# Kernel optimization log

Hardware: AMD Instinct MI355X
Metric: run time of the kernel (lower is better)

The kernel has to match this reference:

```python
import jax, jax.numpy as jnp
import numpy as np

N = 500000
TOL = 0.01
ALPHA = 0.1
SLOPE = 0.01
EPS = 1e-10


def smooth_relu(x):
    # 0 for x<0; x^2/2 for 0<=x<1; x-1/2 for x>=1 (C1 smooth ReLU)
    return jnp.where(x < 0, 0.0, jnp.where(x < 1, 0.5 * x * x, x - 0.5))


def leaky_relu(x):
    return jnp.where(x >= 0, x, SLOPE * x)


def _xavier(key, shape):
    fan_out, fan_in = shape
    std = np.sqrt(2.0 / (fan_in + fan_out)).astype(np.float32)
    return jax.random.normal(key, shape, dtype=jnp.float32) * std


def setup_inputs() -> dict:
    key = jax.random.key(0)
    ks = jax.random.split(key, 16)
    inp = {
        'X': jax.random.normal(ks[0], (N, 2), dtype=jnp.float32),
        'Xstable': jnp.zeros((N, 2), dtype=jnp.float32),
        'Vl1_w': _xavier(ks[1], (64, 2)),
        'V2x_w': _xavier(ks[2], (64, 2)),
        'V2z_w': _xavier(ks[3], (64, 64)),
        'V3x_w': _xavier(ks[4], (64, 2)),
        'V3z_w': _xavier(ks[5], (64, 64)),
        'Vfx_w': _xavier(ks[6], (1, 2)),
        'Vfz_w': _xavier(ks[7], (1, 64)),
        'f1_w': _xavier(ks[8], (128, 2)),
        'f1_b': jnp.zeros((128,), dtype=jnp.float32),
        'f2_w': _xavier(ks[9], (128, 128)),
        'f2_b': jnp.zeros((128,), dtype=jnp.float32),
        'f3_w': _xavier(ks[10], (128, 128)),
        'f3_b': jnp.zeros((128,), dtype=jnp.float32),
        'f4_w': _xavier(ks[11], (128, 128)),
        'f4_b': jnp.zeros((128,), dtype=jnp.float32),
        'f5_w': _xavier(ks[12], (128, 128)),
        'f5_b': jnp.zeros((128,), dtype=jnp.float32),
        'ff_w': _xavier(ks[13], (2, 128)),
        'ff_b': jnp.zeros((2,), dtype=jnp.float32),
    }
    return inp


def _V_forward(X, Xstable, Vl1_w, V2x_w, V2z_w, V3x_w, V3z_w, Vfx_w, Vfz_w):
    d = X - Xstable                                  # [N,2]
    z1 = smooth_relu(d @ Vl1_w.T)                    # [N,64]
    z2 = smooth_relu(d @ V2x_w.T + z1 @ V2z_w.T)     # [N,64]
    z3 = smooth_relu(d @ V3x_w.T + z2 @ V3z_w.T)     # [N,64]
    zf = smooth_relu(d @ Vfx_w.T + z3 @ Vfz_w.T)     # [N,1]
    vsum = TOL * jnp.sum(d * d, axis=1, keepdims=True)
    return smooth_relu(zf) + vsum                    # [N,1]


def _fhat_forward(X, f1_w, f1_b, f2_w, f2_b, f3_w, f3_b, f4_w, f4_b, f5_w, f5_b, ff_w, ff_b):
    h = leaky_relu(X @ f1_w.T + f1_b)
    h = leaky_relu(h @ f2_w.T + f2_b)
    h = leaky_relu(h @ f3_w.T + f3_b)
    h = leaky_relu(h @ f4_w.T + f4_b)
    h = leaky_relu(h @ f5_w.T + f5_b)
    return h @ ff_w.T + ff_b                         # [N,2]


def reference(X, Xstable, Vl1_w, V2x_w, V2z_w, V3x_w, V3z_w, Vfx_w, Vfz_w,
              f1_w, f1_b, f2_w, f2_b, f3_w, f3_b, f4_w, f4_b, f5_w, f5_b, ff_w, ff_b):
    def Vfn(Xv):
        return _V_forward(Xv, Xstable, Vl1_w, V2x_w, V2z_w, V3x_w, V3z_w, Vfx_w, Vfz_w)

    V, pullback = jax.vjp(Vfn, X)
    gradV = pullback(jnp.ones_like(V))[0]            # dV/dX, [N,2]

    f_hat = _fhat_forward(X, f1_w, f1_b, f2_w, f2_b, f3_w, f3_b,
                          f4_w, f4_b, f5_w, f5_b, ff_w, ff_b)

    Vnorm = jnp.sum(gradV * gradV, axis=1, keepdims=True)      # [N,1]
    fh_V = jnp.sum(f_hat * gradV, axis=1, keepdims=True)       # [N,1]
    f_mul = jax.nn.relu(fh_V + ALPHA * V) / (Vnorm + EPS)      # [N,1]
    f = f_hat - gradV * f_mul                                  # [N,2]
    return f
```

## Files before the change

### kernel.cpp

```cpp
#include <hip/hip_runtime.h>


typedef _Float16 v2h __attribute__((ext_vector_type(2)));
typedef __fp16   v2hf __attribute__((ext_vector_type(2)));
typedef _Float16 v4h __attribute__((ext_vector_type(4)));
typedef _Float16 v8h __attribute__((ext_vector_type(8)));
typedef float    v4f __attribute__((ext_vector_type(4)));

__device__ __forceinline__ v2h cvt_pk(float a, float b){
  v2hf r = __builtin_amdgcn_cvt_pkrtz(a, b);
  union { v2hf f; v2h h; } u; u.f = r;
  return u.h;
}

#define NPTS 500000
#define FH_BLK  ((NPTS + 127) / 128)
#define VN_BLK  ((NPTS + 127) / 128)
#define FUSED_GRID (FH_BLK + VN_BLK)

#define OFF_FW    0
#define OFF_V2Z   65536
#define OFF_V3Z   69632
#define OFF_V2ZT  73728
#define OFF_V3ZT  77824
#define OFF_VL1T  81920
#define OFF_V2XT  82048
#define OFF_V3XT  82176
#define OFF_VFZ   82304
#define OFF_FFW   82368
#define OFF_F1W   82624
#define W16_DATA  82880
#define W16_TOTAL (W16_DATA + 2048)

__device__ __align__(16) _Float16 g_w16[W16_TOTAL];
__device__ __align__(16) float    g_fh[NPTS * 2];
__device__ __align__(16) float4   g_grad[NPTS];

#if defined(__has_builtin)
#if __has_builtin(__builtin_amdgcn_fdot2)
#define FDOT2(a,b,c) __builtin_amdgcn_fdot2((a),(b),(c),false)
#endif
#endif
#ifndef FDOT2
__device__ __forceinline__ float fdot2_fb(v2h a, v2h b, float c){
  return fmaf((float)a.x, (float)b.x, fmaf((float)a.y, (float)b.y, c));
}
#define FDOT2(a,b,c) fdot2_fb((a),(b),(c))
#endif

__device__ __forceinline__ float srelu(float x){
  float c = fminf(fmaxf(x, 0.f), 1.f);
  return c * fmaf(-0.5f, c, x);
}
__device__ __forceinline__ float sreluD(float x){
  return fminf(fmaxf(x, 0.f), 1.f);
}
__device__ __forceinline__ float sreluD_from_z(float z){
  return fminf(sqrtf(2.f * z), 1.f);
}
__device__ __forceinline__ float dot8(v8h a, v8h b, float s){
  const v2h* ap = (const v2h*)&a;
  const v2h* bp = (const v2h*)&b;
  s = FDOT2(ap[0], bp[0], s);
  s = FDOT2(ap[1], bp[1], s);
  s = FDOT2(ap[2], bp[2], s);
  s = FDOT2(ap[3], bp[3], s);
  return s;
}

__device__ __forceinline__ v2h lrelu_pk(float a, float b){
  v2h x = cvt_pk(a, b);
  v2h m = x * (v2h){(_Float16)0.01f, (_Float16)0.01f};
  return __builtin_elementwise_max(x, m);
}
__device__ __forceinline__ v2h srelu_pk(float a, float b){
  v2h x = cvt_pk(a, b);
  const v2h z0 = (v2h){(_Float16)0.f, (_Float16)0.f};
  const v2h o1 = (v2h){(_Float16)1.f, (_Float16)1.f};
  const v2h hf = (v2h){(_Float16)0.5f, (_Float16)0.5f};
  v2h c = __builtin_elementwise_min(__builtin_elementwise_max(x, z0), o1);
  v2h t = x - c * hf;
  return c * t;
}

__global__ __launch_bounds__(256) void prep_kernel(
  const float* __restrict__ f2w, const float* __restrict__ f3w,
  const float* __restrict__ f4w, const float* __restrict__ f5w,
  const float* __restrict__ V2z, const float* __restrict__ V3z,
  const float* __restrict__ Vl1, const float* __restrict__ V2x,
  const float* __restrict__ V3x, const float* __restrict__ Vfz,
  const float* __restrict__ ffw, const float* __restrict__ f1w)
{
  const int i = blockIdx.x * 256 + threadIdx.x;
  if (i >= W16_TOTAL) return;
  if (i >= W16_DATA){ g_w16[i] = (_Float16)0.f; return; }
  float v;
  if (i < 65536){
    const float* W[4] = {f2w, f3w, f4w, f5w};
    v = W[i >> 14][i & 16383];
  } else if (i < 69632)  v = V2z[i - 65536];
  else if (i < 73728)    v = V3z[i - 69632];
  else if (i < 77824){ int r = i - 73728; v = V2z[(r & 63)*64 + (r >> 6)]; }
  else if (i < 81920){ int r = i - 77824; v = V3z[(r & 63)*64 + (r >> 6)]; }
  else if (i < 82048){ int r = i - 81920; v = Vl1[(r & 63)*2 + (r >> 6)]; }
  else if (i < 82176){ int r = i - 82048; v = V2x[(r & 63)*2 + (r >> 6)]; }
  else if (i < 82304){ int r = i - 82176; v = V3x[(r & 63)*2 + (r >> 6)]; }
  else if (i < 82368)    v = Vfz[i - 82304];
  else if (i < 82624)    v = ffw[i - 82368];
  else                   v = f1w[i - 82624];
  g_w16[i] = (_Float16)v;
}

__device__ __forceinline__ void fh_layer(_Float16* H,
    const _Float16* __restrict__ Wl, const float* __restrict__ Bp,
    int w, int lm, int q)
{
  v4f acc[2][8];
#pragma unroll
  for (int mt = 0; mt < 2; ++mt)
#pragma unroll
    for (int nt = 0; nt < 8; ++nt) acc[mt][nt] = (v4f){0.f,0.f,0.f,0.f};

#pragma unroll
  for (int kt = 0; kt < 4; ++kt){
    const int sw = ((kt*4 + q) ^ lm) << 3;
    v8h A0 = *(const v8h*)(Wl + (w*32      + lm)*128 + kt*32 + q*8);
    v8h A1 = *(const v8h*)(Wl + (w*32 + 16 + lm)*128 + kt*32 + q*8);
#pragma unroll
    for (int nt = 0; nt < 8; ++nt){
      v8h B = *(const v8h*)(H + (nt*16 + lm)*128 + sw);
      acc[0][nt] = __builtin_amdgcn_mfma_f32_16x16x32_f16(A0, B, acc[0][nt], 0,0,0);
      acc[1][nt] = __builtin_amdgcn_mfma_f32_16x16x32_f16(A1, B, acc[1][nt], 0,0,0);
    }
  }
  __syncthreads();
#pragma unroll
  for (int mt = 0; mt < 2; ++mt){
    const int o0 = w*32 + mt*16 + q*4;
    const v4f bv = *(const v4f*)(Bp + o0);
    const int coff = (((o0 >> 3) ^ lm) << 3) + (o0 & 7);
#pragma unroll
    for (int nt = 0; nt < 8; ++nt){
      v4h hv;
      *(v2h*)&hv       = lrelu_pk(acc[mt][nt][0] + bv[0], acc[mt][nt][1] + bv[1]);
      *((v2h*)&hv + 1) = lrelu_pk(acc[mt][nt][2] + bv[2], acc[mt][nt][3] + bv[3]);
      *(v4h*)(H + (nt*16 + lm)*128 + coff) = hv;
    }
  }
  __syncthreads();
}

__device__ __forceinline__ void fhat_body(int b, _Float16* H,
  const float* __restrict__ X,
  const float* __restrict__ f1b, const float* __restrict__ f2b,
  const float* __restrict__ f3b, const float* __restrict__ f4b,
  const float* __restrict__ f5b, const float* __restrict__ ffb)
{
  const int t  = threadIdx.x;
  const int w  = t >> 6;
  const int l  = t & 63;
  const int lm = l & 15;
  const int q  = l >> 4;

  {
    const int r = t >> 1, hf = t & 1, rsw = r & 15;
    int g = b*128 + r; if (g > NPTS-1) g = NPTS-1;
    const float2 xv = *(const float2*)(X + g*2);
    v2h xh; xh.x = (_Float16)xv.x; xh.y = (_Float16)xv.y;
#pragma unroll
    for (int c8 = 0; c8 < 8; ++c8){
      const int c = hf*8 + c8;
      const v4f b0 = *(const v4f*)(f1b + c*8);
      const v4f b1 = *(const v4f*)(f1b + c*8 + 4);
      float vv[8];
#pragma unroll
      for (int j = 0; j < 8; ++j){
        const v2h wv = *(const v2h*)(g_w16 + OFF_F1W + (c*8 + j)*2);
        const float bb = (j < 4) ? b0[j] : b1[j-4];
        vv[j] = FDOT2(xh, wv, bb);
      }
      v8h hv;
#pragma unroll
      for (int j2 = 0; j2 < 4; ++j2)
        ((v2h*)&hv)[j2] = lrelu_pk(vv[2*j2], vv[2*j2+1]);
      *(v8h*)(H + r*128 + ((c ^ rsw) << 3)) = hv;
    }
  }
  __syncthreads();

  fh_layer(H, g_w16 + OFF_FW,         f2b, w, lm, q);
  fh_layer(H, g_w16 + OFF_FW + 16384, f3b, w, lm, q);
  fh_layer(H, g_w16 + OFF_FW + 32768, f4b, w, lm, q);
  fh_layer(H, g_w16 + OFF_FW + 49152, f5b, w, lm, q);

  {
    const int r = t >> 1, c = t & 1, rsw = r & 15;
    float s = ffb[c];
    const v8h* wf = (const v8h*)(g_w16 + OFF_FFW + c*128);
#pragma unroll
    for (int ck = 0; ck < 16; ++ck){
      v8h h = *(const v8h*)(H + r*128 + ((ck ^ rsw) << 3));
      s = dot8(h, wf[ck], s);
    }
    const int row = b*128 + r;
    if (row < NPTS) g_fh[row*2 + c] = s;
  }
}

__device__ __forceinline__ void vfwd2_l2(_Float16* zoutA, _Float16* zoutB,
    const _Float16* __restrict__ Wz,
    const _Float16* __restrict__ WxT,
    const _Float16* __restrict__ Wl1T,
    float dA0, float dA1, float dB0, float dB1, int lm, int q)
{
  v4f accA[4], accB[4];
#pragma unroll
  for (int mt = 0; mt < 4; ++mt){
    accA[mt] = (v4f){0.f,0.f,0.f,0.f};
    accB[mt] = (v4f){0.f,0.f,0.f,0.f};
  }
  const int rs = lm & 7;
#pragma unroll
  for (int kt = 0; kt < 2; ++kt){
    v8h w0 = *(const v8h*)(Wl1T + kt*32 + q*8);
    v8h w1 = *(const v8h*)(Wl1T + 64 + kt*32 + q*8);
    v8h BA, BB;
#pragma unroll
    for (int j2 = 0; j2 < 4; ++j2){
      const float a0 = (float)w0[2*j2  ], a1 = (float)w0[2*j2+1];
      const float c0 = (float)w1[2*j2  ], c1 = (float)w1[2*j2+1];
      ((v2h*)&BA)[j2] = srelu_pk(fmaf(dA0,a0,dA1*c0), fmaf(dA0,a1,dA1*c1));
      ((v2h*)&BB)[j2] = srelu_pk(fmaf(dB0,a0,dB1*c0), fmaf(dB0,a1,dB1*c1));
    }
#pragma unroll
    for (int mt = 0; mt < 4; ++mt){
      v8h A = *(const v8h*)(Wz + (mt*16 + lm)*64 + kt*32 + q*8);
      accA[mt] = __builtin_amdgcn_mfma_f32_16x16x32_f16(A, BA, accA[mt], 0,0,0);
      accB[mt] = __builtin_amdgcn_mfma_f32_16x16x32_f16(A, BB, accB[mt], 0,0,0);
    }
  }
#pragma unroll
  for (int mt = 0; mt < 4; ++mt){
    const int o0 = mt*16 + q*4;
    const int off = (((o0 >> 3) ^ rs) << 3) + (o0 & 7);
    float vA[4], vB[4];
#pragma unroll
    for (int reg = 0; reg < 4; ++reg){
      const float wx0 = (float)WxT[o0 + reg];
      const float wx1 = (float)WxT[64 + o0 + reg];
      vA[reg] = accA[mt][reg] + wx0*dA0 + wx1*dA1;
      vB[reg] = accB[mt][reg] + wx0*dB0 + wx1*dB1;
    }
    v4h hA, hB;
    *(v2h*)&hA       = srelu_pk(vA[0], vA[1]);
    *((v2h*)&hA + 1) = srelu_pk(vA[2], vA[3]);
    *(v2h*)&hB       = srelu_pk(vB[0], vB[1]);
    *((v2h*)&hB + 1) = srelu_pk(vB[2], vB[3]);
    *(v4h*)(zoutA + lm*64 + off) = hA;
    *(v4h*)(zoutB + lm*64 + off) = hB;
  }
}

__device__ __forceinline__ void vfwd2(const _Float16* zinA, _Float16* zoutA,
    const _Float16* zinB, _Float16* zoutB,
    const _Float16* __restrict__ Wz, const _Float16* __restrict__ WxT,
    float dA0, float dA1, float dB0, float dB1, int lm, int q)
{
  v4f accA[4], accB[4];
#pragma unroll
  for (int mt = 0; mt < 4; ++mt){
    accA[mt] = (v4f){0.f,0.f,0.f,0.f};
    accB[mt] = (v4f){0.f,0.f,0.f,0.f};
  }
  const int rs = lm & 7;
#pragma unroll
  for (int kt = 0; kt < 2; ++kt){
    const int sw = (((kt*4 + q) ^ rs) << 3);
    v8h BA = *(const v8h*)(zinA + lm*64 + sw);
    v8h BB = *(const v8h*)(zinB + lm*64 + sw);
#pragma unroll
    for (int mt = 0; mt < 4; ++mt){
      v8h A = *(const v8h*)(Wz + (mt*16 + lm)*64 + kt*32 + q*8);
      accA[mt] = __builtin_amdgcn_mfma_f32_16x16x32_f16(A, BA, accA[mt], 0,0,0);
      accB[mt] = __builtin_amdgcn_mfma_f32_16x16x32_f16(A, BB, accB[mt], 0,0,0);
    }
  }
#pragma unroll
  for (int mt = 0; mt < 4; ++mt){
    const int o0 = mt*16 + q*4;
    const int off = (((o0 >> 3) ^ rs) << 3) + (o0 & 7);
    float vA[4], vB[4];
#pragma unroll
    for (int reg = 0; reg < 4; ++reg){
      const float wx0 = (float)WxT[o0 + reg];
      const float wx1 = (float)WxT[64 + o0 + reg];
      vA[reg] = accA[mt][reg] + wx0*dA0 + wx1*dA1;
      vB[reg] = accB[mt][reg] + wx0*dB0 + wx1*dB1;
    }
    v4h hA, hB;
    *(v2h*)&hA       = srelu_pk(vA[0], vA[1]);
    *((v2h*)&hA + 1) = srelu_pk(vA[2], vA[3]);
    *(v2h*)&hB       = srelu_pk(vB[0], vB[1]);
    *((v2h*)&hB + 1) = srelu_pk(vB[2], vB[3]);
    *(v4h*)(zoutA + lm*64 + off) = hA;
    *(v4h*)(zoutB + lm*64 + off) = hB;
  }
}

__device__ __forceinline__ void vbwd2(const _Float16* ginA, _Float16* zioA,
    const _Float16* ginB, _Float16* zioB,
    const _Float16* __restrict__ WT, int lm, int q)
{
  v4f accA[4], accB[4];
#pragma unroll
  for (int mt = 0; mt < 4; ++mt){
    accA[mt] = (v4f){0.f,0.f,0.f,0.f};
    accB[mt] = (v4f){0.f,0.f,0.f,0.f};
  }
  const int rs = lm & 7;
#pragma unroll
  for (int kt = 0; kt < 2; ++kt){
    const int sw = (((kt*4 + q) ^ rs) << 3);
    v8h BA = *(const v8h*)(ginA + lm*64 + sw);
    v8h BB = *(const v8h*)(ginB + lm*64 + sw);
#pragma unroll
    for (int mt = 0; mt < 4; ++mt){
      v8h A = *(const v8h*)(WT + (mt*16 + lm)*64 + kt*32 + q*8);
      accA[mt] = __builtin_amdgcn_mfma_f32_16x16x32_f16(A, BA, accA[mt], 0,0,0);
      accB[mt] = __builtin_amdgcn_mfma_f32_16x16x32_f16(A, BB, accB[mt], 0,0,0);
    }
  }
#pragma unroll
  for (int mt = 0; mt < 4; ++mt){
    const int k0 = mt*16 + q*4;
    const int off = (((k0 >> 3) ^ rs) << 3) + (k0 & 7);
    _Float16* pA = zioA + lm*64 + off;
    _Float16* pB = zioB + lm*64 + off;
    v4h zA = *(const v4h*)pA;
    v4h zB = *(const v4h*)pB;
    float sA0 = accA[mt][0] * sreluD_from_z((float)zA[0]);
    float sA1 = accA[mt][1] * sreluD_from_z((float)zA[1]);
    float sA2 = accA[mt][2] * sreluD_from_z((float)zA[2]);
    float sA3 = accA[mt][3] * sreluD_from_z((float)zA[3]);
    float sB0 = accB[mt][0] * sreluD_from_z((float)zB[0]);
    float sB1 = accB[mt][1] * sreluD_from_z((float)zB[1]);
    float sB2 = accB[mt][2] * sreluD_from_z((float)zB[2]);
    float sB3 = accB[mt][3] * sreluD_from_z((float)zB[3]);
    v4h gA, gB;
    *(v2h*)&gA       = cvt_pk(sA0, sA1);
    *((v2h*)&gA + 1) = cvt_pk(sA2, sA3);
    *(v2h*)&gB       = cvt_pk(sB0, sB1);
    *((v2h*)&gB + 1) = cvt_pk(sB2, sB3);
    *(v4h*)pA = gA;
    *(v4h*)pB = gB;
  }
}

__device__ __forceinline__ void vbwd2_l1(_Float16* zioA, _Float16* zioB,
    const _Float16* __restrict__ WT,
    const _Float16* __restrict__ Wl1T,
    float dA0, float dA1, float dB0, float dB1, int lm, int q)
{
  v4f accA[4], accB[4];
#pragma unroll
  for (int mt = 0; mt < 4; ++mt){
    accA[mt] = (v4f){0.f,0.f,0.f,0.f};
    accB[mt] = (v4f){0.f,0.f,0.f,0.f};
  }
  const int rs = lm & 7;
#pragma unroll
  for (int kt = 0; kt < 2; ++kt){
    const int sw = (((kt*4 + q) ^ rs) << 3);
    v8h BA = *(const v8h*)(zioA + lm*64 + sw);
    v8h BB = *(const v8h*)(zioB + lm*64 + sw);
#pragma unroll
    for (int mt = 0; mt < 4; ++mt){
      v8h A = *(const v8h*)(WT + (mt*16 + lm)*64 + kt*32 + q*8);
      accA[mt] = __builtin_amdgcn_mfma_f32_16x16x32_f16(A, BA, accA[mt], 0,0,0);
      accB[mt] = __builtin_amdgcn_mfma_f32_16x16x32_f16(A, BB, accB[mt], 0,0,0);
    }
  }
#pragma unroll
  for (int mt = 0; mt < 4; ++mt){
    const int k0 = mt*16 + q*4;
    const int off = (((k0 >> 3) ^ rs) << 3) + (k0 & 7);
    v4h w0 = *(const v4h*)(Wl1T + k0);
    v4h w1 = *(const v4h*)(Wl1T + 64 + k0);
    float sA[4], sB[4];
#pragma unroll
    for (int reg = 0; reg < 4; ++reg){
      const float a1A = fmaf(dA0, (float)w0[reg], dA1 * (float)w1[reg]);
      const float a1B = fmaf(dB0, (float)w0[reg], dB1 * (float)w1[reg]);
      sA[reg] = accA[mt][reg] * sreluD(a1A);
      sB[reg] = accB[mt][reg] * sreluD(a1B);
    }
    v4h gA, gB;
    *(v2h*)&gA       = cvt_pk(sA[0], sA[1]);
    *((v2h*)&gA + 1) = cvt_pk(sA[2], sA[3]);
    *(v2h*)&gB       = cvt_pk(sB[0], sB[1]);
    *((v2h*)&gB + 1) = cvt_pk(sB[2], sB[3]);
    *(v4h*)(zioA + lm*64 + off) = gA;
    *(v4h*)(zioB + lm*64 + off) = gB;
  }
}

__device__ __forceinline__ void gacc2(v4f& aGA, v4f& aGB,
    const _Float16* __restrict__ WxTbase,
    const _Float16* ZA, const _Float16* ZB, int lm, int q)
{
  const int rs = lm & 7;
#pragma unroll
  for (int kt = 0; kt < 2; ++kt){
    const int sw = (((kt*4 + q) ^ rs) << 3);
    v8h A  = *(const v8h*)(WxTbase + lm*64 + kt*32 + q*8);
    v8h BA = *(const v8h*)(ZA + lm*64 + sw);
    v8h BB = *(const v8h*)(ZB + lm*64 + sw);
    aGA = __builtin_amdgcn_mfma_f32_16x16x32_f16(A, BA, aGA, 0,0,0);
    aGB = __builtin_amdgcn_mfma_f32_16x16x32_f16(A, BB, aGB, 0,0,0);
  }
}

__device__ __forceinline__ void vnet_body2(int b, char* smem,
  const float* __restrict__ X, const float* __restrict__ Xst,
  const float* __restrict__ Vfx)
{
  const int t  = threadIdx.x;
  const int w  = t >> 6;
  const int l  = t & 63;
  const int lm = l & 15;
  const int q  = l >> 4;
  const int rs = lm & 7;

  _Float16* const ZA2 = (_Float16*)(smem + w*8192);
  _Float16* const ZA3 = ZA2 + 1024;
  _Float16* const ZB2 = ZA2 + 2048;
  _Float16* const ZB3 = ZA2 + 3072;

  const int rowA = b*128 + w*32 + lm;
  const int rowB = rowA + 16;
  const int rcA = rowA < NPTS ? rowA : NPTS-1;
  const int rcB = rowB < NPTS ? rowB : NPTS-1;
  const float2 xA = *(const float2*)(X   + rcA*2);
  const float2 sA = *(const float2*)(Xst + rcA*2);
  const float2 xB = *(const float2*)(X   + rcB*2);
  const float2 sB = *(const float2*)(Xst + rcB*2);
  const float dA0 = xA.x - sA.x, dA1 = xA.y - sA.y;
  const float dB0 = xB.x - sB.x, dB1 = xB.y - sB.y;
  const float vfx0 = Vfx[0], vfx1 = Vfx[1];

  vfwd2_l2(ZA2, ZB2, g_w16 + OFF_V2Z, g_w16 + OFF_V2XT, g_w16 + OFF_VL1T,
           dA0, dA1, dB0, dB1, lm, q);
  vfwd2(ZA2, ZA3, ZB2, ZB3, g_w16 + OFF_V3Z, g_w16 + OFF_V3XT,
        dA0, dA1, dB0, dB1, lm, q);

  float VVrA, sfA, VVrB, sfB;
  {
    v4f aSA = (v4f){0.f,0.f,0.f,0.f};
    v4f aSB = (v4f){0.f,0.f,0.f,0.f};
#pragma unroll
    for (int kt = 0; kt < 2; ++kt){
      const int sw = (((kt*4 + q) ^ rs) << 3);
      v8h A  = *(const v8h*)(g_w16 + OFF_VFZ + lm*64 + kt*32 + q*8);
      v8h BA = *(const v8h*)(ZA3 + lm*64 + sw);
      v8h BB = *(const v8h*)(ZB3 + lm*64 + sw);
      aSA = __builtin_amdgcn_mfma_f32_16x16x32_f16(A, BA, aSA, 0,0,0);
      aSB = __builtin_amdgcn_mfma_f32_16x16x32_f16(A, BB, aSB, 0,0,0);
    }
    const float afA = fmaf(vfx0, dA0, fmaf(vfx1, dA1, aSA[0]));
    const float zfA = srelu(afA);
    VVrA = srelu(zfA) + 0.01f * fmaf(dA0, dA0, dA1*dA1);
    sfA  = sreluD(zfA) * sreluD(afA);
    const float afB = fmaf(vfx0, dB0, fmaf(vfx1, dB1, aSB[0]));
    const float zfB = srelu(afB);
    VVrB = srelu(zfB) + 0.01f * fmaf(dB0, dB0, dB1*dB1);
    sfB  = sreluD(zfB) * sreluD(afB);
  }

#pragma unroll
  for (int cc = 0; cc < 2; ++cc){
    const int c = q*2 + cc;
    const int sw = ((c ^ rs) << 3);
    v8h vf = *(const v8h*)(g_w16 + OFF_VFZ + c*8);
    _Float16* pA = ZA3 + lm*64 + sw;
    _Float16* pB = ZB3 + lm*64 + sw;
    v8h zA = *(const v8h*)pA;
    v8h zB = *(const v8h*)pB;
    v8h uA, uB;
#pragma unroll
    for (int j2 = 0; j2 < 4; ++j2){
      float a0 = (float)vf[2*j2  ] * sreluD_from_z((float)zA[2*j2  ]);
      float a1 = (float)vf[2*j2+1] * sreluD_from_z((float)zA[2*j2+1]);
      float b0 = (float)vf[2*j2  ] * sreluD_from_z((float)zB[2*j2  ]);
      float b1 = (float)vf[2*j2+1] * sreluD_from_z((float)zB[2*j2+1]);
      ((v2h*)&uA)[j2] = cvt_pk(a0, a1);
      ((v2h*)&uB)[j2] = cvt_pk(b0, b1);
    }
    *(v8h*)pA = uA;
    *(v8h*)pB = uB;
  }

  v4f aGA = (v4f){0.f,0.f,0.f,0.f};
  v4f aGB = (v4f){0.f,0.f,0.f,0.f};

  gacc2(aGA, aGB, g_w16 + OFF_V3XT, ZA3, ZB3, lm, q);
  vbwd2(ZA3, ZA2, ZB3, ZB2, g_w16 + OFF_V3ZT, lm, q);
  gacc2(aGA, aGB, g_w16 + OFF_V2XT, ZA2, ZB2, lm, q);
  vbwd2_l1(ZA2, ZB2, g_w16 + OFF_V2ZT, g_w16 + OFF_VL1T,
           dA0, dA1, dB0, dB1, lm, q);
  gacc2(aGA, aGB, g_w16 + OFF_VL1T, ZA2, ZB2, lm, q);

  const float g0A = fmaf(0.02f, dA0, sfA * (vfx0 + aGA[0]));
  const float g1A = fmaf(0.02f, dA1, sfA * (vfx1 + aGA[1]));
  const float g0B = fmaf(0.02f, dB0, sfB * (vfx0 + aGB[0]));
  const float g1B = fmaf(0.02f, dB1, sfB * (vfx1 + aGB[1]));

  if (q == 0){
    if (rowA < NPTS) g_grad[rowA] = make_float4(g0A, g1A, VVrA, 0.f);
    if (rowB < NPTS) g_grad[rowB] = make_float4(g0B, g1B, VVrB, 0.f);
  }
}

__global__ __launch_bounds__(256, 4) void fused_kernel(
  const float* __restrict__ X, const float* __restrict__ Xst,
  const float* __restrict__ Vfx,
  const float* __restrict__ f1b, const float* __restrict__ f2b,
  const float* __restrict__ f3b, const float* __restrict__ f4b,
  const float* __restrict__ f5b, const float* __restrict__ ffb)
{
  __shared__ __align__(16) char smem[32768];
  const int g = blockIdx.x;
  if ((g & 1) == 0){
    fhat_body(g >> 1, (_Float16*)smem, X, f1b, f2b, f3b, f4b, f5b, ffb);
  } else {
    vnet_body2(g >> 1, smem, X, Xst, Vfx);
  }
}

__global__ __launch_bounds__(256) void combine_kernel(float* __restrict__ out)
{
  const int idx = blockIdx.x * 256 + threadIdx.x;
  const int i0 = idx * 2;
  if (i0 >= NPTS) return;
  const float4 fh2 = *(const float4*)(g_fh + i0*2);
  const float4 ga = g_grad[i0];
  const float4 gb = g_grad[i0 + 1];
  float4 o;
  {
    const float Vn  = fmaf(ga.x, ga.x, ga.y*ga.y);
    const float num = fmaf(0.1f, ga.z, fmaf(fh2.x, ga.x, fh2.y*ga.y));
    const float fm  = fmaxf(num, 0.f) / (Vn + 1e-10f);
    o.x = fmaf(-ga.x, fm, fh2.x);
    o.y = fmaf(-ga.y, fm, fh2.y);
  }
  {
    const float Vn  = fmaf(gb.x, gb.x, gb.y*gb.y);
    const float num = fmaf(0.1f, gb.z, fmaf(fh2.z, gb.x, fh2.w*gb.y));
    const float fm  = fmaxf(num, 0.f) / (Vn + 1e-10f);
    o.z = fmaf(-gb.x, fm, fh2.z);
    o.w = fmaf(-gb.y, fm, fh2.w);
  }
  *(float4*)(out + i0*2) = o;
}

extern "C" void kernel_launch(void* const* d_in, const int* in_sizes, int n_in,
                              void* d_out, int out_size, void* d_ws, size_t ws_size,
                              hipStream_t stream)
{
  (void)d_ws; (void)ws_size; (void)n_in; (void)in_sizes; (void)out_size;
  const float* X   = (const float*)d_in[0];
  const float* Xst = (const float*)d_in[1];
  const float* Vl1 = (const float*)d_in[2];
  const float* V2x = (const float*)d_in[3];
  const float* V2z = (const float*)d_in[4];
  const float* V3x = (const float*)d_in[5];
  const float* V3z = (const float*)d_in[6];
  const float* Vfx = (const float*)d_in[7];
  const float* Vfz = (const float*)d_in[8];
  const float* f1w = (const float*)d_in[9];
  const float* f1b = (const float*)d_in[10];
  const float* f2w = (const float*)d_in[11];
  const float* f2b = (const float*)d_in[12];
  const float* f3w = (const float*)d_in[13];
  const float* f3b = (const float*)d_in[14];
  const float* f4w = (const float*)d_in[15];
  const float* f4b = (const float*)d_in[16];
  const float* f5w = (const float*)d_in[17];
  const float* f5b = (const float*)d_in[18];
  const float* ffw = (const float*)d_in[19];
  const float* ffb = (const float*)d_in[20];

  prep_kernel<<<(W16_TOTAL + 255)/256, 256, 0, stream>>>(
      f2w, f3w, f4w, f5w, V2z, V3z, Vl1, V2x, V3x, Vfz, ffw, f1w);
  fused_kernel<<<FUSED_GRID, 256, 0, stream>>>(
      X, Xst, Vfx, f1b, f2b, f3b, f4b, f5b, ffb);
  combine_kernel<<<(NPTS/2 + 255)/256, 256, 0, stream>>>((float*)d_out);
}
```

Measured before the change: 308.6 us.

## Make fhat MLP wave-private with per-wave row tiles and MFMA input/output layers

Restructures the fhat MLP so each wave owns 32 rows and computes all 128 output features, keeping activations in a private smem slice and dropping all block-level barriers between layers. The first layer becomes an MFMA over a zero-padded K=32 weight copy, and the final 128->2 projection also uses MFMA, replacing the scalar fdot2 loops. In exchange each wave now streams the full weight matrix from global/cache per layer, which raises weight traffic and register pressure, and the final layer uses a padded weight tile.

```diff
diff --git a/kernel.cpp b/kernel.cpp
--- a/kernel.cpp
+++ b/kernel.cpp
@@ -15,8 +15,7 @@
 
 #define NPTS 500000
 #define FH_BLK  ((NPTS + 127) / 128)
-#define VN_BLK  ((NPTS + 127) / 128)
-#define FUSED_GRID (FH_BLK + VN_BLK)
+#define FUSED_GRID (FH_BLK * 2)
 
 #define OFF_FW    0
 #define OFF_V2Z   65536
@@ -29,7 +28,8 @@
 #define OFF_VFZ   82304
 #define OFF_FFW   82368
 #define OFF_F1W   82624
-#define W16_DATA  82880
+#define OFF_F1P   82880
+#define W16_DATA  86976
 #define W16_TOTAL (W16_DATA + 2048)
 
 __device__ __align__(16) _Float16 g_w16[W16_TOTAL];
@@ -57,15 +57,6 @@
 }
 __device__ __forceinline__ float sreluD_from_z(float z){
   return fminf(sqrtf(2.f * z), 1.f);
-}
-__device__ __forceinline__ float dot8(v8h a, v8h b, float s){
-  const v2h* ap = (const v2h*)&a;
-  const v2h* bp = (const v2h*)&b;
-  s = FDOT2(ap[0], bp[0], s);
-  s = FDOT2(ap[1], bp[1], s);
-  s = FDOT2(ap[2], bp[2], s);
-  s = FDOT2(ap[3], bp[3], s);
-  return s;
 }
 
 __device__ __forceinline__ v2h lrelu_pk(float a, float b){
@@ -107,50 +98,49 @@
   else if (i < 82304){ int r = i - 82176; v = V3x[(r & 63)*2 + (r >> 6)]; }
   else if (i < 82368)    v = Vfz[i - 82304];
   else if (i < 82624)    v = ffw[i - 82368];
-  else                   v = f1w[i - 82624];
+  else if (i < 82880)    v = f1w[i - 82624];
+  else { int r = i - 82880; int k = r & 31; v = (k < 2) ? f1w[(r >> 5)*2 + k] : 0.f; }
   g_w16[i] = (_Float16)v;
 }
 
-__device__ __forceinline__ void fh_layer(_Float16* H,
+__device__ __forceinline__ void fh_layer_w(_Float16* Hw,
     const _Float16* __restrict__ Wl, const float* __restrict__ Bp,
-    int w, int lm, int q)
-{
-  v4f acc[2][8];
-#pragma unroll
-  for (int mt = 0; mt < 2; ++mt)
-#pragma unroll
-    for (int nt = 0; nt < 8; ++nt) acc[mt][nt] = (v4f){0.f,0.f,0.f,0.f};
-
+    int lm, int q)
+{
+  v4f acc[8][2];
+#pragma unroll
+  for (int mt = 0; mt < 8; ++mt){
+    acc[mt][0] = (v4f){0.f,0.f,0.f,0.f};
+    acc[mt][1] = (v4f){0.f,0.f,0.f,0.f};
+  }
 #pragma unroll
   for (int kt = 0; kt < 4; ++kt){
     const int sw = ((kt*4 + q) ^ lm) << 3;
-    v8h A0 = *(const v8h*)(Wl + (w*32      + lm)*128 + kt*32 + q*8);
-    v8h A1 = *(const v8h*)(Wl + (w*32 + 16 + lm)*128 + kt*32 + q*8);
-#pragma unroll
-    for (int nt = 0; nt < 8; ++nt){
-      v8h B = *(const v8h*)(H + (nt*16 + lm)*128 + sw);
-      acc[0][nt] = __builtin_amdgcn_mfma_f32_16x16x32_f16(A0, B, acc[0][nt], 0,0,0);
-      acc[1][nt] = __builtin_amdgcn_mfma_f32_16x16x32_f16(A1, B, acc[1][nt], 0,0,0);
-    }
-  }
-  __syncthreads();
-#pragma unroll
-  for (int mt = 0; mt < 2; ++mt){
-    const int o0 = w*32 + mt*16 + q*4;
+    v8h B0 = *(const v8h*)(Hw + lm*128 + sw);
+    v8h B1 = *(const v8h*)(Hw + (16 + lm)*128 + sw);
+#pragma unroll
+    for (int mt = 0; mt < 8; ++mt){
+      v8h A = *(const v8h*)(Wl + (mt*16 + lm)*128 + kt*32 + q*8);
+      acc[mt][0] = __builtin_amdgcn_mfma_f32_16x16x32_f16(A, B0, acc[mt][0], 0,0,0);
+      acc[mt][1] = __builtin_amdgcn_mfma_f32_16x16x32_f16(A, B1, acc[mt][1], 0,0,0);
+    }
+  }
+#pragma unroll
+  for (int mt = 0; mt < 8; ++mt){
+    const int o0 = mt*16 + q*4;
     const v4f bv = *(const v4f*)(Bp + o0);
     const int coff = (((o0 >> 3) ^ lm) << 3) + (o0 & 7);
-#pragma unroll
-    for (int nt = 0; nt < 8; ++nt){
-      v4h hv;
-      *(v2h*)&hv       = lrelu_pk(acc[mt][nt][0] + bv[0], acc[mt][nt][1] + bv[1]);
-      *((v2h*)&hv + 1) = lrelu_pk(acc[mt][nt][2] + bv[2], acc[mt][nt][3] + bv[3]);
-      *(v4h*)(H + (nt*16 + lm)*128 + coff) = hv;
-    }
-  }
-  __syncthreads();
-}
-
-__device__ __forceinline__ void fhat_body(int b, _Float16* H,
+    v4h h0, h1;
+    *(v2h*)&h0       = lrelu_pk(acc[mt][0][0] + bv[0], acc[mt][0][1] + bv[1]);
+    *((v2h*)&h0 + 1) = lrelu_pk(acc[mt][0][2] + bv[2], acc[mt][0][3] + bv[3]);
+    *(v2h*)&h1       = lrelu_pk(acc[mt][1][0] + bv[0], acc[mt][1][1] + bv[1]);
+    *((v2h*)&h1 + 1) = lrelu_pk(acc[mt][1][2] + bv[2], acc[mt][1][3] + bv[3]);
+    *(v4h*)(Hw + lm*128 + coff)        = h0;
+    *(v4h*)(Hw + (16 + lm)*128 + coff) = h1;
+  }
+}
+
+__device__ __forceinline__ void fhat_body(int b, char* smem,
   const float* __restrict__ X,
   const float* __restrict__ f1b, const float* __restrict__ f2b,
   const float* __restrict__ f3b, const float* __restrict__ f4b,
@@ -161,49 +151,71 @@
   const int l  = t & 63;
   const int lm = l & 15;
   const int q  = l >> 4;
+  _Float16* const Hw = (_Float16*)smem + w*4096;
+  const int row0 = b*128 + w*32;
 
   {
-    const int r = t >> 1, hf = t & 1, rsw = r & 15;
-    int g = b*128 + r; if (g > NPTS-1) g = NPTS-1;
-    const float2 xv = *(const float2*)(X + g*2);
-    v2h xh; xh.x = (_Float16)xv.x; xh.y = (_Float16)xv.y;
-#pragma unroll
-    for (int c8 = 0; c8 < 8; ++c8){
-      const int c = hf*8 + c8;
-      const v4f b0 = *(const v4f*)(f1b + c*8);
-      const v4f b1 = *(const v4f*)(f1b + c*8 + 4);
-      float vv[8];
-#pragma unroll
-      for (int j = 0; j < 8; ++j){
-        const v2h wv = *(const v2h*)(g_w16 + OFF_F1W + (c*8 + j)*2);
-        const float bb = (j < 4) ? b0[j] : b1[j-4];
-        vv[j] = FDOT2(xh, wv, bb);
-      }
-      v8h hv;
-#pragma unroll
-      for (int j2 = 0; j2 < 4; ++j2)
-        ((v2h*)&hv)[j2] = lrelu_pk(vv[2*j2], vv[2*j2+1]);
-      *(v8h*)(H + r*128 + ((c ^ rsw) << 3)) = hv;
-    }
-  }
-  __syncthreads();
-
-  fh_layer(H, g_w16 + OFF_FW,         f2b, w, lm, q);
-  fh_layer(H, g_w16 + OFF_FW + 16384, f3b, w, lm, q);
-  fh_layer(H, g_w16 + OFF_FW + 32768, f4b, w, lm, q);
-  fh_layer(H, g_w16 + OFF_FW + 49152, f5b, w, lm, q);
+    int r0 = row0 + lm;      if (r0 > NPTS-1) r0 = NPTS-1;
+    int r1 = row0 + 16 + lm; if (r1 > NPTS-1) r1 = NPTS-1;
+    const float2 x0 = *(const float2*)(X + r0*2);
+    const float2 x1 = *(const float2*)(X + r1*2);
+    v8h Bx0 = (v8h){(_Float16)0.f,(_Float16)0.f,(_Float16)0.f,(_Float16)0.f,
+                    (_Float16)0.f,(_Float16)0.f,(_Float16)0.f,(_Float16)0.f};
+    v8h Bx1 = Bx0;
+    if (q == 0){
+      Bx0[0] = (_Float16)x0.x; Bx0[1] = (_Float16)x0.y;
+      Bx1[0] = (_Float16)x1.x; Bx1[1] = (_Float16)x1.y;
+    }
+    v4f acc[8][2];
+#pragma unroll
+    for (int mt = 0; mt < 8; ++mt){
+      acc[mt][0] = (v4f){0.f,0.f,0.f,0.f};
+      acc[mt][1] = (v4f){0.f,0.f,0.f,0.f};
+    }
+#pragma unroll
+    for (int mt = 0; mt < 8; ++mt){
+      v8h A = *(const v8h*)(g_w16 + OFF_F1P + (mt*16 + lm)*32 + q*8);
+      acc[mt][0] = __builtin_amdgcn_mfma_f32_16x16x32_f16(A, Bx0, acc[mt][0], 0,0,0);
+      acc[mt][1] = __builtin_amdgcn_mfma_f32_16x16x32_f16(A, Bx1, acc[mt][1], 0,0,0);
+    }
+#pragma unroll
+    for (int mt = 0; mt < 8; ++mt){
+      const int o0 = mt*16 + q*4;
+      const v4f bv = *(const v4f*)(f1b + o0);
+      const int coff = (((o0 >> 3) ^ lm) << 3) + (o0 & 7);
+      v4h h0, h1;
+      *(v2h*)&h0       = lrelu_pk(acc[mt][0][0] + bv[0], acc[mt][0][1] + bv[1]);
+      *((v2h*)&h0 + 1) = lrelu_pk(acc[mt][0][2] + bv[2], acc[mt][0][3] + bv[3]);
+      *(v2h*)&h1       = lrelu_pk(acc[mt][1][0] + bv[0], acc[mt][1][1] + bv[1]);
+      *((v2h*)&h1 + 1) = lrelu_pk(acc[mt][1][2] + bv[2], acc[mt][1][3] + bv[3]);
+      *(v4h*)(Hw + lm*128 + coff)        = h0;
+      *(v4h*)(Hw + (16 + lm)*128 + coff) = h1;
+    }
+  }
+
+  fh_layer_w(Hw, g_w16 + OFF_FW,         f2b, lm, q);
+  fh_layer_w(Hw, g_w16 + OFF_FW + 16384, f3b, lm, q);
+  fh_layer_w(Hw, g_w16 + OFF_FW + 32768, f4b, lm, q);
+  fh_layer_w(Hw, g_w16 + OFF_FW + 49152, f5b, lm, q);
 
   {
-    const int r = t >> 1, c = t & 1, rsw = r & 15;
-    float s = ffb[c];
-    const v8h* wf = (const v8h*)(g_w16 + OFF_FFW + c*128);
-#pragma unroll
-    for (int ck = 0; ck < 16; ++ck){
-      v8h h = *(const v8h*)(H + r*128 + ((ck ^ rsw) << 3));
-      s = dot8(h, wf[ck], s);
-    }
-    const int row = b*128 + r;
-    if (row < NPTS) g_fh[row*2 + c] = s;
+    v4f a0 = (v4f){0.f,0.f,0.f,0.f};
+    v4f a1 = (v4f){0.f,0.f,0.f,0.f};
+#pragma unroll
+    for (int kt = 0; kt < 4; ++kt){
+      const int sw = ((kt*4 + q) ^ lm) << 3;
+      v8h A  = *(const v8h*)(g_w16 + OFF_FFW + lm*128 + kt*32 + q*8);
+      v8h B0 = *(const v8h*)(Hw + lm*128 + sw);
+      v8h B1 = *(const v8h*)(Hw + (16 + lm)*128 + sw);
+      a0 = __builtin_amdgcn_mfma_f32_16x16x32_f16(A, B0, a0, 0,0,0);
+      a1 = __builtin_amdgcn_mfma_f32_16x16x32_f16(A, B1, a1, 0,0,0);
+    }
+    if (q == 0){
+      const float fb0 = ffb[0], fb1 = ffb[1];
+      const int r0 = row0 + lm, r1 = row0 + 16 + lm;
+      if (r0 < NPTS) *(float2*)(g_fh + r0*2) = make_float2(a0[0] + fb0, a0[1] + fb1);
+      if (r1 < NPTS) *(float2*)(g_fh + r1*2) = make_float2(a1[0] + fb0, a1[1] + fb1);
+    }
   }
 }
 
@@ -530,7 +542,7 @@
   __shared__ __align__(16) char smem[32768];
   const int g = blockIdx.x;
   if ((g & 1) == 0){
-    fhat_body(g >> 1, (_Float16*)smem, X, f1b, f2b, f3b, f4b, f5b, ffb);
+    fhat_body(g >> 1, smem, X, f1b, f2b, f3b, f4b, f5b, ffb);
   } else {
     vnet_body2(g >> 1, smem, X, Xst, Vfx);
   }
```

Result: slower. 623.5 us (+102.1%).
